# Performance work log

Measured on AMD Instinct MI355X. Metric: run time of the kernel, lower is better.

The kernel has to match this reference:

```python
import jax, jax.numpy as jnp
import numpy as np

B, S, H, I, E, TOPK = 2, 2048, 1024, 2816, 7, 2


def setup_inputs() -> dict:
    key = jax.random.key(0)
    ks = jax.random.split(key, 8)
    sh = 1.0 / np.sqrt(H).astype(np.float32)   # fan-in scale for H->I projections
    si = 1.0 / np.sqrt(I).astype(np.float32)   # fan-in scale for I->H projections
    return {
        "x": jax.random.normal(ks[0], (B, S, H), jnp.float32),
        "Wg_shared": jax.random.normal(ks[1], (I, H), jnp.float32) * sh,
        "Wu_shared": jax.random.normal(ks[2], (I, H), jnp.float32) * sh,
        "Wd_shared": jax.random.normal(ks[3], (H, I), jnp.float32) * si,
        "Wg": jax.random.normal(ks[4], (E, I, H), jnp.float32) * sh,
        "Wu": jax.random.normal(ks[5], (E, I, H), jnp.float32) * sh,
        "Wd": jax.random.normal(ks[6], (E, H, I), jnp.float32) * si,
        "Wr": jax.random.normal(ks[7], (E, H), jnp.float32) * sh,
    }


def reference(x, Wg_shared, Wu_shared, Wd_shared, Wg, Wu, Wd, Wr):
    # Shared expert: SwiGLU MLP applied to every token.
    sg = jnp.einsum('bsh,ih->bsi', x, Wg_shared)
    su = jnp.einsum('bsh,ih->bsi', x, Wu_shared)
    shared_out = jnp.einsum('bsi,hi->bsh', jax.nn.silu(sg) * su, Wd_shared)

    # Router: top-k over logits, softmax over the selected k logits.
    router_logits = jnp.einsum('bsh,eh->bse', x, Wr)          # [B,S,E]
    rw, sel = jax.lax.top_k(router_logits, TOPK)              # [B,S,K]
    rw = jax.nn.softmax(rw, axis=-1)
    # Per-expert combine weight (equivalent to the scatter-built mask * weight).
    comb = jnp.sum(rw[..., None] * jax.nn.one_hot(sel, E, dtype=x.dtype), axis=2)  # [B,S,E]

    # Torch module runs every expert densely on every token, then masks.
    g = jnp.einsum('bsh,eih->ebsi', x, Wg)                    # [E,B,S,I]
    u = jnp.einsum('bsh,eih->ebsi', x, Wu)
    y = jnp.einsum('ebsi,ehi->ebsh', jax.nn.silu(g) * u, Wd)  # [E,B,S,H]
    moe_out = jnp.einsum('ebsh,bse->bsh', y, comb)

    return shared_out + moe_out, router_logits
```

## Files before the change

### kernel.cpp

```cpp
#include <hip/hip_runtime.h>
#include <hip/hip_bf16.h>

#define NTOK 4096
#define HH 1024
#define II 2816
#define EE 7
#define SHARED_BASE 8192
#define NSLOT 12288

typedef __bf16 bf16x8 __attribute__((ext_vector_type(8)));
typedef __bf16 bf16x4 __attribute__((ext_vector_type(4)));
typedef float  f32x4v __attribute__((ext_vector_type(4)));

typedef const __attribute__((address_space(1))) void* gas_ptr;
typedef __attribute__((address_space(3))) void* las_ptr;
__device__ __forceinline__ void load16_lds(const void* g, void* l) {
    __builtin_amdgcn_global_load_lds((gas_ptr)g, (las_ptr)l, 16, 0, 0);
}

__global__ void cvt_x(const float* __restrict__ x, __bf16* __restrict__ xb) {
    int i = blockIdx.x * blockDim.x + threadIdx.x;
    const f32x4v* xv = (const f32x4v*)x;
    bf16x4* ov = (bf16x4*)xb;
    int base = i * 4;
#pragma unroll
    for (int j = 0; j < 4; j++) {
        f32x4v f = xv[base + j];
        bf16x4 b;
        b[0] = (__bf16)f[0]; b[1] = (__bf16)f[1];
        b[2] = (__bf16)f[2]; b[3] = (__bf16)f[3];
        ov[base + j] = b;
    }
}

__global__ void cvt_w6(const float* __restrict__ Wg, const float* __restrict__ Wu,
                       const float* __restrict__ Wgs, const float* __restrict__ Wus,
                       const float* __restrict__ Wd, const float* __restrict__ Wds,
                       __bf16* __restrict__ wgu, __bf16* __restrict__ wgus,
                       __bf16* __restrict__ wdb, __bf16* __restrict__ wdsb) {
    const int y = blockIdx.y;
    const int H4 = HH / 4;
    const int stride = gridDim.x * blockDim.x;
    int idx0 = blockIdx.x * blockDim.x + threadIdx.x;
    if (y < 2) {
        const f32x4v* sv = (const f32x4v*)(y == 0 ? Wg : Wu);
        const int add = y * 16;
        const int n4 = EE * II * H4;
        for (int idx = idx0; idx < n4; idx += stride) {
            int h4 = idx & (H4 - 1);
            int row = idx >> 8;
            int e = row / II, i = row - e * II;
            int crow = e * 2 * II + ((i >> 4) * 32) + (i & 15) + add;
            f32x4v f = sv[idx];
            bf16x4 b;
            b[0] = (__bf16)f[0]; b[1] = (__bf16)f[1];
            b[2] = (__bf16)f[2]; b[3] = (__bf16)f[3];
            ((bf16x4*)wgu)[crow * H4 + h4] = b;
        }
    } else if (y < 4) {
        const f32x4v* sv = (const f32x4v*)(y == 2 ? Wgs : Wus);
        const int add = (y - 2) * 16;
        const int n4 = II * H4;
        for (int idx = idx0; idx < n4; idx += stride) {
            int h4 = idx & (H4 - 1);
            int i = idx >> 8;
            int crow = ((i >> 4) * 32) + (i & 15) + add;
            f32x4v f = sv[idx];
            bf16x4 b;
            b[0] = (__bf16)f[0]; b[1] = (__bf16)f[1];
            b[2] = (__bf16)f[2]; b[3] = (__bf16)f[3];
            ((bf16x4*)wgus)[crow * H4 + h4] = b;
        }
    } else {
        const f32x4v* sv = (const f32x4v*)(y == 4 ? Wd : Wds);
        bf16x4* dv = (bf16x4*)(y == 4 ? wdb : wdsb);
        const int n4 = (y == 4 ? EE : 1) * HH * II / 4;
        for (int idx = idx0; idx < n4; idx += stride) {
            f32x4v f = sv[idx];
            bf16x4 b;
            b[0] = (__bf16)f[0]; b[1] = (__bf16)f[1];
            b[2] = (__bf16)f[2]; b[3] = (__bf16)f[3];
            dv[idx] = b;
        }
    }
}

__global__ void router_k(const float* __restrict__ x, const float* __restrict__ Wr,
                         float* __restrict__ logits, int* __restrict__ counts,
                         int* __restrict__ sel, float* __restrict__ wtop,
                         int* __restrict__ tlist, float* __restrict__ wlist) {
    int wave = threadIdx.x >> 6;
    int lane = threadIdx.x & 63;
    int t = blockIdx.x * 4 + wave;
    const float* xr = x + (size_t)t * HH;
    double acc[EE];
#pragma unroll
    for (int e = 0; e < EE; e++) acc[e] = 0.0;
    for (int j = 0; j < 16; j++) {
        int h = lane + j * 64;
        double xv = (double)xr[h];
#pragma unroll
        for (int e = 0; e < EE; e++) acc[e] += xv * (double)Wr[e * HH + h];
    }
#pragma unroll
    for (int e = 0; e < EE; e++) {
        for (int off = 32; off > 0; off >>= 1) acc[e] += __shfl_down(acc[e], off, 64);
    }
    if (lane == 0) {
        int e0 = 0;
        for (int e = 1; e < EE; e++) if (acc[e] > acc[e0]) e0 = e;
        int e1 = -1;
        for (int e = 0; e < EE; e++) {
            if (e == e0) continue;
            if (e1 < 0 || acc[e] > acc[e1]) e1 = e;
        }
        double w1 = exp(acc[e1] - acc[e0]);
        double s = 1.0 + w1;
        for (int e = 0; e < EE; e++) logits[(size_t)t * EE + e] = (float)acc[e];
        sel[2 * t] = e0; sel[2 * t + 1] = e1;
        wtop[2 * t] = (float)(1.0 / s); wtop[2 * t + 1] = (float)(w1 / s);
        atomicAdd(&counts[e0], 1);
        atomicAdd(&counts[e1], 1);
        tlist[SHARED_BASE + t] = t;
        wlist[SHARED_BASE + t] = 1.0f;
    }
}

__global__ void finalize_k(const int* __restrict__ counts, int* __restrict__ cursor,
                           int* __restrict__ nlist, int* __restrict__ offs) {
    if (threadIdx.x == 0 && blockIdx.x == 0) {
        int o = 0;
        for (int e = 0; e < EE; e++) {
            offs[e] = o; cursor[e] = o; nlist[e] = counts[e];
            o += counts[e];
        }
        offs[EE] = SHARED_BASE;
        nlist[EE] = NTOK;
        cursor[EE] = SHARED_BASE;
    }
}

__global__ void scatter_k(const int* __restrict__ sel, const float* __restrict__ wtop,
                          int* __restrict__ cursor, int* __restrict__ tlist,
                          float* __restrict__ wlist, int* __restrict__ inv) {
    int t = blockIdx.x * blockDim.x + threadIdx.x;
    if (t >= NTOK) return;
#pragma unroll
    for (int j = 0; j < 2; j++) {
        int e = sel[2 * t + j];
        int slot = atomicAdd(&cursor[e], 1);
        tlist[slot] = t;
        wlist[slot] = wtop[2 * t + j];
        inv[2 * t + j] = slot;
    }
}

__global__ __launch_bounds__(256, 3) void gateup_gu(
        const __bf16* __restrict__ Wgu, const __bf16* __restrict__ Wgus,
        const __bf16* __restrict__ xb, __bf16* __restrict__ hbuf,
        const int* __restrict__ nlist, const int* __restrict__ offs,
        const int* __restrict__ tlist) {
    const int e = blockIdx.z;
    const int ne = nlist[e];
    const int bx = blockIdx.x;
    const int nt = (bx & 7) + 8 * (bx >> 8);
    const int mt = (bx >> 3) & 31;
    if (nt >= (2 * II) / 128) return;
    if (mt * 128 >= ne) return;
    const int base = offs[e];
    const __bf16* w = (e < EE) ? Wgu + (size_t)e * 2 * II * HH : Wgus;

    __shared__ __bf16 As[128 * 32];
    __shared__ __bf16 Bs[128 * 32];

    const int tid = threadIdx.x;
    const int r0 = tid >> 2;
    const int c  = tid & 3;
    const int cs = (c ^ ((r0 >> 1) & 3)) * 8;
    const int cl0 = min(mt * 128 + r0, ne - 1);
    const int cl1 = min(mt * 128 + r0 + 64, ne - 1);
    const __bf16* aptr0 = xb + (size_t)tlist[base + cl0] * HH + cs;
    const __bf16* aptr1 = xb + (size_t)tlist[base + cl1] * HH + cs;
    const __bf16* bptr0 = w + (size_t)(nt * 128 + r0) * HH + cs;
    const __bf16* bptr1 = w + (size_t)(nt * 128 + r0 + 64) * HH + cs;
    __bf16* ldsA0 = &As[tid * 8];
    __bf16* ldsA1 = &As[64 * 32 + tid * 8];
    __bf16* ldsB0 = &Bs[tid * 8];
    __bf16* ldsB1 = &Bs[64 * 32 + tid * 8];

    const int wid = tid >> 6, lane = tid & 63;
    const int wm = wid >> 1, wn = wid & 1;
    const int l16 = lane & 15, quad = lane >> 4;
    const int qsw = (quad ^ ((l16 >> 1) & 3)) * 8;

    f32x4v acc[4][4];
#pragma unroll
    for (int i = 0; i < 4; i++)
#pragma unroll
        for (int j = 0; j < 4; j++) acc[i][j] = (f32x4v)0.0f;

    for (int k0 = 0; k0 < HH; k0 += 32) {
        __syncthreads();
        load16_lds(aptr0 + k0, ldsA0);
        load16_lds(aptr1 + k0, ldsA1);
        load16_lds(bptr0 + k0, ldsB0);
        load16_lds(bptr1 + k0, ldsB1);
        __syncthreads();
        bf16x8 a[4];
#pragma unroll
        for (int i = 0; i < 4; i++)
            a[i] = *(const bf16x8*)&As[(wm * 64 + i * 16 + l16) * 32 + qsw];
#pragma unroll
        for (int j = 0; j < 4; j++) {
            bf16x8 b = *(const bf16x8*)&Bs[(wn * 64 + j * 16 + l16) * 32 + qsw];
#pragma unroll
            for (int i = 0; i < 4; i++)
                acc[i][j] = __builtin_amdgcn_mfma_f32_16x16x32_bf16(a[i], b, acc[i][j], 0, 0, 0);
        }
    }
#pragma unroll
    for (int i = 0; i < 4; i++) {
        const int mrow = mt * 128 + wm * 64 + i * 16 + quad * 4;
#pragma unroll
        for (int r = 0; r < 4; r++) {
            const int slot = mrow + r;
            if (slot < ne) {
                __bf16* hrow = hbuf + (size_t)(base + slot) * II + nt * 64 + wn * 32 + l16;
#pragma unroll
                for (int jj = 0; jj < 2; jj++) {
                    float g = acc[i][2 * jj][r], u = acc[i][2 * jj + 1][r];
                    float sgl = g / (1.0f + __expf(-g));
                    hrow[jj * 16] = (__bf16)(sgl * u);
                }
            }
        }
    }
}

__global__ __launch_bounds__(256, 3) void down_y(
        const __bf16* __restrict__ Wd, const __bf16* __restrict__ Wds,
        const __bf16* __restrict__ hbuf, float* __restrict__ ybuf,
        const int* __restrict__ nlist, const int* __restrict__ offs,
        const int* __restrict__ tlist, const float* __restrict__ wlist) {
    const int e = blockIdx.z;
    const int ne = nlist[e];
    const int bx = blockIdx.x;
    const int nt = bx & 7;
    const int mt = bx >> 3;
    if (mt * 128 >= ne) return;
    const int base = offs[e];
    const __bf16* wd = (e < EE) ? Wd + (size_t)e * HH * II : Wds;

    __shared__ __bf16 As[128 * 32];
    __shared__ __bf16 Bs[128 * 32];

    const int tid = threadIdx.x;
    const int r0 = tid >> 2;
    const int c  = tid & 3;
    const int cs = (c ^ ((r0 >> 1) & 3)) * 8;
    const int cl0 = min(mt * 128 + r0, ne - 1);
    const int cl1 = min(mt * 128 + r0 + 64, ne - 1);
    const __bf16* aptr0 = hbuf + (size_t)(base + cl0) * II + cs;
    const __bf16* aptr1 = hbuf + (size_t)(base + cl1) * II + cs;
    const __bf16* bptr0 = wd + (size_t)(nt * 128 + r0) * II + cs;
    const __bf16* bptr1 = wd + (size_t)(nt * 128 + r0 + 64) * II + cs;
    __bf16* ldsA0 = &As[tid * 8];
    __bf16* ldsA1 = &As[64 * 32 + tid * 8];
    __bf16* ldsB0 = &Bs[tid * 8];
    __bf16* ldsB1 = &Bs[64 * 32 + tid * 8];

    const int wid = tid >> 6, lane = tid & 63;
    const int wm = wid >> 1, wn = wid & 1;
    const int l16 = lane & 15, quad = lane >> 4;
    const int qsw = (quad ^ ((l16 >> 1) & 3)) * 8;

    f32x4v acc[4][4];
#pragma unroll
    for (int i = 0; i < 4; i++)
#pragma unroll
        for (int j = 0; j < 4; j++) acc[i][j] = (f32x4v)0.0f;

    for (int k0 = 0; k0 < II; k0 += 32) {
        __syncthreads();
        load16_lds(aptr0 + k0, ldsA0);
        load16_lds(aptr1 + k0, ldsA1);
        load16_lds(bptr0 + k0, ldsB0);
        load16_lds(bptr1 + k0, ldsB1);
        __syncthreads();
        bf16x8 a[4];
#pragma unroll
        for (int i = 0; i < 4; i++)
            a[i] = *(const bf16x8*)&As[(wm * 64 + i * 16 + l16) * 32 + qsw];
#pragma unroll
        for (int j = 0; j < 4; j++) {
            bf16x8 b = *(const bf16x8*)&Bs[(wn * 64 + j * 16 + l16) * 32 + qsw];
#pragma unroll
            for (int i = 0; i < 4; i++)
                acc[i][j] = __builtin_amdgcn_mfma_f32_16x16x32_bf16(a[i], b, acc[i][j], 0, 0, 0);
        }
    }
#pragma unroll
    for (int i = 0; i < 4; i++) {
        const int mrow = mt * 128 + wm * 64 + i * 16 + quad * 4;
#pragma unroll
        for (int r = 0; r < 4; r++) {
            const int slot = mrow + r;
            if (slot < ne) {
                const int idx = base + slot;
                const float w = wlist[idx];
                float* orow = ybuf + (size_t)idx * HH + nt * 128 + wn * 64 + l16;
#pragma unroll
                for (int j = 0; j < 4; j++)
                    orow[j * 16] = w * acc[i][j][r];
            }
        }
    }
}

__global__ void combine_k(const float* __restrict__ ybuf, const int* __restrict__ inv,
                          float* __restrict__ out) {
    int idx = blockIdx.x * blockDim.x + threadIdx.x;
    int t = idx >> 8, h4 = idx & 255;
    const f32x4v* y0 = (const f32x4v*)(ybuf + (size_t)inv[2 * t] * HH);
    const f32x4v* y1 = (const f32x4v*)(ybuf + (size_t)inv[2 * t + 1] * HH);
    const f32x4v* ys = (const f32x4v*)(ybuf + (size_t)(SHARED_BASE + t) * HH);
    f32x4v r = y0[h4] + y1[h4] + ys[h4];
    ((f32x4v*)(out + (size_t)t * HH))[h4] = r;
}

extern "C" void kernel_launch(void* const* d_in, const int* in_sizes, int n_in,
                              void* d_out, int out_size, void* d_ws, size_t ws_size,
                              hipStream_t stream) {
    const float* x   = (const float*)d_in[0];
    const float* Wgs = (const float*)d_in[1];
    const float* Wus = (const float*)d_in[2];
    const float* Wds = (const float*)d_in[3];
    const float* Wg  = (const float*)d_in[4];
    const float* Wu  = (const float*)d_in[5];
    const float* Wd  = (const float*)d_in[6];
    const float* Wr  = (const float*)d_in[7];
    float* out = (float*)d_out;
    float* logits = out + (size_t)NTOK * HH;

    const size_t HB  = (size_t)NSLOT * II * 2;
    const size_t XB  = (size_t)NTOK * HH * 2;
    const size_t WEB = (size_t)EE * II * HH * 2;
    const size_t WSB = (size_t)II * HH * 2;

    char* ws = (char*)d_ws;
    __bf16* hbuf = (__bf16*)ws;
    __bf16* xb   = (__bf16*)(ws + HB);
    __bf16* wgu  = (__bf16*)(ws + HB + XB);
    float*  ybuf = (float*)wgu;
    __bf16* wdb  = (__bf16*)(ws + HB + XB + 2 * WEB);
    __bf16* wgus = (__bf16*)(ws + HB + XB + 3 * WEB);
    __bf16* wdsb = (__bf16*)(ws + HB + XB + 3 * WEB + 2 * WSB);
    char* meta   = ws + HB + XB + 3 * WEB + 3 * WSB;
    int* counts = (int*)meta;
    int* cursor = counts + 8;
    int* nlist  = cursor + 8;
    int* offs   = nlist + 8;
    int* sel    = offs + 8;
    int* tlist  = sel + 2 * NTOK;
    float* wtop = (float*)(tlist + NSLOT);
    float* wlist = wtop + 2 * NTOK;
    int* inv    = (int*)(wlist + NSLOT);

    hipMemsetAsync(counts, 0, 8 * sizeof(int), stream);

    cvt_x<<<1024, 256, 0, stream>>>(x, xb);
    cvt_w6<<<dim3(1024, 6), 256, 0, stream>>>(Wg, Wu, Wgs, Wus, Wd, Wds,
                                              wgu, wgus, wdb, wdsb);
    router_k<<<NTOK / 4, 256, 0, stream>>>(x, Wr, logits, counts, sel, wtop, tlist, wlist);
    finalize_k<<<1, 64, 0, stream>>>(counts, cursor, nlist, offs);
    scatter_k<<<NTOK / 256, 256, 0, stream>>>(sel, wtop, cursor, tlist, wlist, inv);
    gateup_gu<<<dim3(1536, 1, EE + 1), 256, 0, stream>>>(wgu, wgus, xb, hbuf,
                                                         nlist, offs, tlist);
    down_y<<<dim3(256, 1, EE + 1), 256, 0, stream>>>(wdb, wdsb, hbuf, ybuf,
                                                     nlist, offs, tlist, wlist);
    combine_k<<<NTOK, 256, 0, stream>>>(ybuf, inv, out);
}
```

Before: 770.9 us.

## Double-buffer gate/up GEMM with 256x256 tiles and fuse prep kernels

Rewrites the gate/up grouped GEMM to use 256x256 output tiles with K=64 steps, 512 threads, and double-buffered LDS fed by async global-to-LDS loads. Manual vmcnt waits, barriers and MFMA priority hints let the next tile's loads overlap the current tile's math. The router, x conversion and weight conversion kernels are also merged into one launch with 8-wide bf16 stores. The aim is fewer launches, more data reuse per tile and hidden memory latency, at the cost of 128KB of LDS, occupancy of one block per CU, and more wasted work on partial M tiles.

```diff
diff --git a/kernel.cpp b/kernel.cpp
--- a/kernel.cpp
+++ b/kernel.cpp
@@ -18,111 +18,99 @@
     __builtin_amdgcn_global_load_lds((gas_ptr)g, (las_ptr)l, 16, 0, 0);
 }
 
-__global__ void cvt_x(const float* __restrict__ x, __bf16* __restrict__ xb) {
-    int i = blockIdx.x * blockDim.x + threadIdx.x;
-    const f32x4v* xv = (const f32x4v*)x;
-    bf16x4* ov = (bf16x4*)xb;
-    int base = i * 4;
-#pragma unroll
-    for (int j = 0; j < 4; j++) {
-        f32x4v f = xv[base + j];
-        bf16x4 b;
-        b[0] = (__bf16)f[0]; b[1] = (__bf16)f[1];
-        b[2] = (__bf16)f[2]; b[3] = (__bf16)f[3];
-        ov[base + j] = b;
-    }
-}
-
-__global__ void cvt_w6(const float* __restrict__ Wg, const float* __restrict__ Wu,
+#define VMCNT(n) asm volatile("s_waitcnt vmcnt(" #n ")" ::: "memory")
+#define LGKM0    asm volatile("s_waitcnt lgkmcnt(0)" ::: "memory")
+
+__device__ __forceinline__ bf16x8 cvt8(f32x4v f0, f32x4v f1) {
+    bf16x8 b;
+    b[0] = (__bf16)f0[0]; b[1] = (__bf16)f0[1]; b[2] = (__bf16)f0[2]; b[3] = (__bf16)f0[3];
+    b[4] = (__bf16)f1[0]; b[5] = (__bf16)f1[1]; b[6] = (__bf16)f1[2]; b[7] = (__bf16)f1[3];
+    return b;
+}
+
+__global__ void prep_k(const float* __restrict__ x, const float* __restrict__ Wr,
+                       const float* __restrict__ Wg, const float* __restrict__ Wu,
                        const float* __restrict__ Wgs, const float* __restrict__ Wus,
                        const float* __restrict__ Wd, const float* __restrict__ Wds,
-                       __bf16* __restrict__ wgu, __bf16* __restrict__ wgus,
-                       __bf16* __restrict__ wdb, __bf16* __restrict__ wdsb) {
+                       __bf16* __restrict__ xb, __bf16* __restrict__ wgu,
+                       __bf16* __restrict__ wgus, __bf16* __restrict__ wdb,
+                       __bf16* __restrict__ wdsb,
+                       float* __restrict__ logits, int* __restrict__ counts,
+                       int* __restrict__ sel, float* __restrict__ wtop,
+                       int* __restrict__ tlist, float* __restrict__ wlist) {
     const int y = blockIdx.y;
-    const int H4 = HH / 4;
+    const int tid = threadIdx.x;
     const int stride = gridDim.x * blockDim.x;
-    int idx0 = blockIdx.x * blockDim.x + threadIdx.x;
-    if (y < 2) {
-        const f32x4v* sv = (const f32x4v*)(y == 0 ? Wg : Wu);
-        const int add = y * 16;
-        const int n4 = EE * II * H4;
-        for (int idx = idx0; idx < n4; idx += stride) {
-            int h4 = idx & (H4 - 1);
-            int row = idx >> 8;
-            int e = row / II, i = row - e * II;
-            int crow = e * 2 * II + ((i >> 4) * 32) + (i & 15) + add;
-            f32x4v f = sv[idx];
-            bf16x4 b;
-            b[0] = (__bf16)f[0]; b[1] = (__bf16)f[1];
-            b[2] = (__bf16)f[2]; b[3] = (__bf16)f[3];
-            ((bf16x4*)wgu)[crow * H4 + h4] = b;
-        }
-    } else if (y < 4) {
-        const f32x4v* sv = (const f32x4v*)(y == 2 ? Wgs : Wus);
+    int idx0 = blockIdx.x * blockDim.x + tid;
+
+    if (y == 0) {
+        int wave = tid >> 6, lane = tid & 63;
+        int t = blockIdx.x * 4 + wave;
+        const float* xr = x + (size_t)t * HH;
+        double acc[EE];
+#pragma unroll
+        for (int e = 0; e < EE; e++) acc[e] = 0.0;
+        for (int j = 0; j < 16; j++) {
+            int h = lane + j * 64;
+            double xv = (double)xr[h];
+#pragma unroll
+            for (int e = 0; e < EE; e++) acc[e] += xv * (double)Wr[e * HH + h];
+        }
+#pragma unroll
+        for (int e = 0; e < EE; e++) {
+            for (int off = 32; off > 0; off >>= 1) acc[e] += __shfl_down(acc[e], off, 64);
+        }
+        if (lane == 0) {
+            int e0 = 0;
+            for (int e = 1; e < EE; e++) if (acc[e] > acc[e0]) e0 = e;
+            int e1 = -1;
+            for (int e = 0; e < EE; e++) {
+                if (e == e0) continue;
+                if (e1 < 0 || acc[e] > acc[e1]) e1 = e;
+            }
+            double w1 = exp(acc[e1] - acc[e0]);
+            double s = 1.0 + w1;
+            for (int e = 0; e < EE; e++) logits[(size_t)t * EE + e] = (float)acc[e];
+            sel[2 * t] = e0; sel[2 * t + 1] = e1;
+            wtop[2 * t] = (float)(1.0 / s); wtop[2 * t + 1] = (float)(w1 / s);
+            atomicAdd(&counts[e0], 1);
+            atomicAdd(&counts[e1], 1);
+            tlist[SHARED_BASE + t] = t;
+            wlist[SHARED_BASE + t] = 1.0f;
+        }
+    } else if (y == 1) {
+        const f32x4v* xv = (const f32x4v*)x;
+        bf16x8* ov = (bf16x8*)xb;
+        int n8 = NTOK * HH / 8;
+        for (int i = idx0; i < n8; i += stride)
+            ov[i] = cvt8(xv[2 * i], xv[2 * i + 1]);
+    } else if (y <= 3) {
+        const f32x4v* sv = (const f32x4v*)(y == 2 ? Wg : Wu);
         const int add = (y - 2) * 16;
-        const int n4 = II * H4;
-        for (int idx = idx0; idx < n4; idx += stride) {
-            int h4 = idx & (H4 - 1);
-            int i = idx >> 8;
-            int crow = ((i >> 4) * 32) + (i & 15) + add;
-            f32x4v f = sv[idx];
-            bf16x4 b;
-            b[0] = (__bf16)f[0]; b[1] = (__bf16)f[1];
-            b[2] = (__bf16)f[2]; b[3] = (__bf16)f[3];
-            ((bf16x4*)wgus)[crow * H4 + h4] = b;
+        const int n8 = EE * II * (HH / 8);
+        for (int idx = idx0; idx < n8; idx += stride) {
+            int h8 = idx & 127, row = idx >> 7;
+            int e2 = row / II, i2 = row - e2 * II;
+            int crow = e2 * 2 * II + (i2 >> 4) * 32 + (i2 & 15) + add;
+            bf16x8 b = cvt8(sv[row * 256 + h8 * 2], sv[row * 256 + h8 * 2 + 1]);
+            *(bf16x8*)&wgu[(size_t)crow * HH + h8 * 8] = b;
+        }
+    } else if (y <= 5) {
+        const f32x4v* sv = (const f32x4v*)(y == 4 ? Wgs : Wus);
+        const int add = (y - 4) * 16;
+        const int n8 = II * (HH / 8);
+        for (int idx = idx0; idx < n8; idx += stride) {
+            int h8 = idx & 127, i2 = idx >> 7;
+            int crow = (i2 >> 4) * 32 + (i2 & 15) + add;
+            bf16x8 b = cvt8(sv[i2 * 256 + h8 * 2], sv[i2 * 256 + h8 * 2 + 1]);
+            *(bf16x8*)&wgus[(size_t)crow * HH + h8 * 8] = b;
         }
     } else {
-        const f32x4v* sv = (const f32x4v*)(y == 4 ? Wd : Wds);
-        bf16x4* dv = (bf16x4*)(y == 4 ? wdb : wdsb);
-        const int n4 = (y == 4 ? EE : 1) * HH * II / 4;
-        for (int idx = idx0; idx < n4; idx += stride) {
-            f32x4v f = sv[idx];
-            bf16x4 b;
-            b[0] = (__bf16)f[0]; b[1] = (__bf16)f[1];
-            b[2] = (__bf16)f[2]; b[3] = (__bf16)f[3];
-            dv[idx] = b;
-        }
-    }
-}
-
-__global__ void router_k(const float* __restrict__ x, const float* __restrict__ Wr,
-                         float* __restrict__ logits, int* __restrict__ counts,
-                         int* __restrict__ sel, float* __restrict__ wtop,
-                         int* __restrict__ tlist, float* __restrict__ wlist) {
-    int wave = threadIdx.x >> 6;
-    int lane = threadIdx.x & 63;
-    int t = blockIdx.x * 4 + wave;
-    const float* xr = x + (size_t)t * HH;
-    double acc[EE];
-#pragma unroll
-    for (int e = 0; e < EE; e++) acc[e] = 0.0;
-    for (int j = 0; j < 16; j++) {
-        int h = lane + j * 64;
-        double xv = (double)xr[h];
-#pragma unroll
-        for (int e = 0; e < EE; e++) acc[e] += xv * (double)Wr[e * HH + h];
-    }
-#pragma unroll
-    for (int e = 0; e < EE; e++) {
-        for (int off = 32; off > 0; off >>= 1) acc[e] += __shfl_down(acc[e], off, 64);
-    }
-    if (lane == 0) {
-        int e0 = 0;
-        for (int e = 1; e < EE; e++) if (acc[e] > acc[e0]) e0 = e;
-        int e1 = -1;
-        for (int e = 0; e < EE; e++) {
-            if (e == e0) continue;
-            if (e1 < 0 || acc[e] > acc[e1]) e1 = e;
-        }
-        double w1 = exp(acc[e1] - acc[e0]);
-        double s = 1.0 + w1;
-        for (int e = 0; e < EE; e++) logits[(size_t)t * EE + e] = (float)acc[e];
-        sel[2 * t] = e0; sel[2 * t + 1] = e1;
-        wtop[2 * t] = (float)(1.0 / s); wtop[2 * t + 1] = (float)(w1 / s);
-        atomicAdd(&counts[e0], 1);
-        atomicAdd(&counts[e1], 1);
-        tlist[SHARED_BASE + t] = t;
-        wlist[SHARED_BASE + t] = 1.0f;
+        const f32x4v* sv = (const f32x4v*)(y == 6 ? Wd : Wds);
+        bf16x8* dv = (bf16x8*)(y == 6 ? wdb : wdsb);
+        const int n8 = (y == 6 ? EE : 1) * HH * (II / 8);
+        for (int idx = idx0; idx < n8; idx += stride)
+            dv[idx] = cvt8(sv[2 * idx], sv[2 * idx + 1]);
     }
 }
 
@@ -155,77 +143,113 @@
     }
 }
 
-__global__ __launch_bounds__(256, 3) void gateup_gu(
+__global__ __launch_bounds__(512, 1) void gugemm(
         const __bf16* __restrict__ Wgu, const __bf16* __restrict__ Wgus,
         const __bf16* __restrict__ xb, __bf16* __restrict__ hbuf,
         const int* __restrict__ nlist, const int* __restrict__ offs,
         const int* __restrict__ tlist) {
     const int e = blockIdx.z;
     const int ne = nlist[e];
-    const int bx = blockIdx.x;
-    const int nt = (bx & 7) + 8 * (bx >> 8);
-    const int mt = (bx >> 3) & 31;
-    if (nt >= (2 * II) / 128) return;
-    if (mt * 128 >= ne) return;
+    const int nt = blockIdx.x % 22;
+    const int mt = blockIdx.x / 22;
+    if (mt * 256 >= ne) return;
     const int base = offs[e];
     const __bf16* w = (e < EE) ? Wgu + (size_t)e * 2 * II * HH : Wgus;
 
-    __shared__ __bf16 As[128 * 32];
-    __shared__ __bf16 Bs[128 * 32];
+    __shared__ __bf16 sm[2][2][256 * 64];
 
     const int tid = threadIdx.x;
-    const int r0 = tid >> 2;
-    const int c  = tid & 3;
-    const int cs = (c ^ ((r0 >> 1) & 3)) * 8;
-    const int cl0 = min(mt * 128 + r0, ne - 1);
-    const int cl1 = min(mt * 128 + r0 + 64, ne - 1);
-    const __bf16* aptr0 = xb + (size_t)tlist[base + cl0] * HH + cs;
-    const __bf16* aptr1 = xb + (size_t)tlist[base + cl1] * HH + cs;
-    const __bf16* bptr0 = w + (size_t)(nt * 128 + r0) * HH + cs;
-    const __bf16* bptr1 = w + (size_t)(nt * 128 + r0 + 64) * HH + cs;
-    __bf16* ldsA0 = &As[tid * 8];
-    __bf16* ldsA1 = &As[64 * 32 + tid * 8];
-    __bf16* ldsB0 = &Bs[tid * 8];
-    __bf16* ldsB1 = &Bs[64 * 32 + tid * 8];
+    const __bf16* ap[4]; const __bf16* bp[4];
+    int dstoff[4];
+#pragma unroll
+    for (int l = 0; l < 4; l++) {
+        int idx = tid + l * 512;
+        int row = idx >> 3, ck = idx & 7;
+        int cks = (ck ^ (row & 7)) * 8;
+        int cl = min(mt * 256 + row, ne - 1);
+        ap[l] = xb + (size_t)tlist[base + cl] * HH + cks;
+        bp[l] = w + (size_t)(nt * 256 + row) * HH + cks;
+        dstoff[l] = idx * 8;
+    }
+
+#define STAGE(bufi, kof) do {                                          \
+    _Pragma("unroll")                                                  \
+    for (int l = 0; l < 4; l++)                                        \
+        load16_lds(ap[l] + (kof), &sm[bufi][0][dstoff[l]]);            \
+    _Pragma("unroll")                                                  \
+    for (int l = 0; l < 4; l++)                                        \
+        load16_lds(bp[l] + (kof), &sm[bufi][1][dstoff[l]]);            \
+} while (0)
 
     const int wid = tid >> 6, lane = tid & 63;
-    const int wm = wid >> 1, wn = wid & 1;
+    const int wm = wid >> 2, wn = wid & 3;
     const int l16 = lane & 15, quad = lane >> 4;
-    const int qsw = (quad ^ ((l16 >> 1) & 3)) * 8;
-
-    f32x4v acc[4][4];
-#pragma unroll
-    for (int i = 0; i < 4; i++)
+    const int rsw = l16 & 7;
+    const int ckof0 = (quad ^ rsw) * 8;
+    const int ckof1 = ((4 + quad) ^ rsw) * 8;
+    const int arow = wm * 128 + l16;
+    const int brow = wn * 64 + l16;
+
+    f32x4v acc[8][4];
+#pragma unroll
+    for (int i = 0; i < 8; i++)
 #pragma unroll
         for (int j = 0; j < 4; j++) acc[i][j] = (f32x4v)0.0f;
 
-    for (int k0 = 0; k0 < HH; k0 += 32) {
-        __syncthreads();
-        load16_lds(aptr0 + k0, ldsA0);
-        load16_lds(aptr1 + k0, ldsA1);
-        load16_lds(bptr0 + k0, ldsB0);
-        load16_lds(bptr1 + k0, ldsB1);
-        __syncthreads();
-        bf16x8 a[4];
-#pragma unroll
-        for (int i = 0; i < 4; i++)
-            a[i] = *(const bf16x8*)&As[(wm * 64 + i * 16 + l16) * 32 + qsw];
-#pragma unroll
-        for (int j = 0; j < 4; j++) {
-            bf16x8 b = *(const bf16x8*)&Bs[(wn * 64 + j * 16 + l16) * 32 + qsw];
-#pragma unroll
-            for (int i = 0; i < 4; i++)
-                acc[i][j] = __builtin_amdgcn_mfma_f32_16x16x32_bf16(a[i], b, acc[i][j], 0, 0, 0);
-        }
-    }
-#pragma unroll
-    for (int i = 0; i < 4; i++) {
-        const int mrow = mt * 128 + wm * 64 + i * 16 + quad * 4;
+#define COMPUTE(bufi) do {                                                        \
+    bf16x8 bfr[4][2];                                                             \
+    _Pragma("unroll")                                                             \
+    for (int j = 0; j < 4; j++) {                                                 \
+        bfr[j][0] = *(const bf16x8*)&sm[bufi][1][(brow + j * 16) * 64 + ckof0];   \
+        bfr[j][1] = *(const bf16x8*)&sm[bufi][1][(brow + j * 16) * 64 + ckof1];   \
+    }                                                                             \
+    _Pragma("unroll")                                                             \
+    for (int h = 0; h < 2; h++) {                                                 \
+        bf16x8 afr[4][2];                                                         \
+        _Pragma("unroll")                                                         \
+        for (int i2 = 0; i2 < 4; i2++) {                                          \
+            int rr = (arow + (h * 4 + i2) * 16) * 64;                             \
+            afr[i2][0] = *(const bf16x8*)&sm[bufi][0][rr + ckof0];                 \
+            afr[i2][1] = *(const bf16x8*)&sm[bufi][0][rr + ckof1];                 \
+        }                                                                         \
+        __builtin_amdgcn_s_setprio(1);                                            \
+        _Pragma("unroll")                                                         \
+        for (int ks = 0; ks < 2; ks++)                                            \
+            _Pragma("unroll")                                                     \
+            for (int j = 0; j < 4; j++)                                           \
+                _Pragma("unroll")                                                 \
+                for (int i2 = 0; i2 < 4; i2++)                                    \
+                    acc[h * 4 + i2][j] = __builtin_amdgcn_mfma_f32_16x16x32_bf16( \
+                        afr[i2][ks], bfr[j][ks], acc[h * 4 + i2][j], 0, 0, 0);    \
+        __builtin_amdgcn_s_setprio(0);                                            \
+    }                                                                             \
+} while (0)
+
+    STAGE(0, 0);
+    for (int t = 0; t < 15; t++) {
+        const int buf = t & 1;
+        STAGE(buf ^ 1, (t + 1) * 64);
+        VMCNT(8);
+        __builtin_amdgcn_s_barrier();
+        __builtin_amdgcn_sched_barrier(0);
+        COMPUTE(buf);
+        LGKM0;
+        __builtin_amdgcn_sched_barrier(0);
+        __builtin_amdgcn_s_barrier();
+    }
+    VMCNT(0);
+    __builtin_amdgcn_s_barrier();
+    __builtin_amdgcn_sched_barrier(0);
+    COMPUTE(1);
+
+#pragma unroll
+    for (int i = 0; i < 8; i++) {
+        const int mrow = mt * 256 + wm * 128 + i * 16 + quad * 4;
 #pragma unroll
         for (int r = 0; r < 4; r++) {
             const int slot = mrow + r;
             if (slot < ne) {
-                __bf16* hrow = hbuf + (size_t)(base + slot) * II + nt * 64 + wn * 32 + l16;
+                __bf16* hrow = hbuf + (size_t)(base + slot) * II + nt * 128 + wn * 32 + l16;
 #pragma unroll
                 for (int jj = 0; jj < 2; jj++) {
                     float g = acc[i][2 * jj][r], u = acc[i][2 * jj + 1][r];
@@ -235,6 +259,8 @@
             }
         }
     }
+#undef STAGE
+#undef COMPUTE
 }
 
 __global__ __launch_bounds__(256, 3) void down_y(
@@ -368,14 +394,13 @@
 
     hipMemsetAsync(counts, 0, 8 * sizeof(int), stream);
 
-    cvt_x<<<1024, 256, 0, stream>>>(x, xb);
-    cvt_w6<<<dim3(1024, 6), 256, 0, stream>>>(Wg, Wu, Wgs, Wus, Wd, Wds,
-                                              wgu, wgus, wdb, wdsb);
-    router_k<<<NTOK / 4, 256, 0, stream>>>(x, Wr, logits, counts, sel, wtop, tlist, wlist);
+    prep_k<<<dim3(1024, 8), 256, 0, stream>>>(x, Wr, Wg, Wu, Wgs, Wus, Wd, Wds,
+                                              xb, wgu, wgus, wdb, wdsb,
+                                              logits, counts, sel, wtop, tlist, wlist);
     finalize_k<<<1, 64, 0, stream>>>(counts, cursor, nlist, offs);
     scatter_k<<<NTOK / 256, 256, 0, stream>>>(sel, wtop, cursor, tlist, wlist, inv);
-    gateup_gu<<<dim3(1536, 1, EE + 1), 256, 0, stream>>>(wgu, wgus, xb, hbuf,
-                                                         nlist, offs, tlist);
+    gugemm<<<dim3(352, 1, EE + 1), 512, 0, stream>>>(wgu, wgus, xb, hbuf,
+                                                     nlist, offs, tlist);
     down_y<<<dim3(256, 1, EE + 1), 256, 0, stream>>>(wdb, wdsb, hbuf, ybuf,
                                                      nlist, offs, tlist, wlist);
     combine_k<<<NTOK, 256, 0, stream>>>(ybuf, inv, out);
```

After: 717.0 us. 1.08x faster.
